# Performance work log

Measured on AMD Instinct MI355X. Metric: run time of the kernel, lower is better.

Reference implementation:

```python
import jax, jax.numpy as jnp
import numpy as np

N_QUBITS = 12
N_LAYERS = 5
OUTPUT_DIM = 4
BATCH = 1024


def _apply_1q(state, U, q, n):
    # state: (B, 2^n) complex; U: (B, 2, 2) per-sample unitary on wire q
    B = state.shape[0]
    s = state.reshape(B, 2 ** q, 2, -1)
    s = jnp.einsum('bik,bakc->baic', U, s)
    return s.reshape(B, -1)


def _cnot(state, c, t, n):
    # CNOT with control wire c, target wire t (wire 0 = most significant bit)
    B = state.shape[0]
    s = state.reshape((B,) + (2,) * n)
    s0 = jax.lax.index_in_dim(s, 0, axis=1 + c, keepdims=True)
    s1 = jax.lax.index_in_dim(s, 1, axis=1 + c, keepdims=True)
    s1 = jnp.flip(s1, axis=1 + t)  # X on target where control = 1
    return jnp.concatenate([s0, s1], axis=1 + c).reshape(B, -1)


def _forward(x, input_weights, theta, output_weights):
    n, L, D = N_QUBITS, N_LAYERS, OUTPUT_DIM
    x = jnp.tanh(x)
    B = x.shape[0]
    # |0...0> initial state, batched
    state = jnp.zeros((B, 2 ** n), jnp.complex64).at[:, 0].set(1.0)
    for l in range(L):
        # data re-uploading: RX(input_weights[l,j] * x[:,j]) on every wire, every layer
        a = input_weights[l][None, :] * x          # (B, n) RX angles
        b = theta[l, :, 0]                          # (n,) RY angles
        c = theta[l, :, 1]                          # (n,) RZ angles
        ca = jnp.cos(a / 2).astype(jnp.complex64)
        sa = jnp.sin(a / 2).astype(jnp.complex64)
        Rx = jnp.stack([jnp.stack([ca, -1j * sa], -1),
                        jnp.stack([-1j * sa, ca], -1)], -2)  # (B, n, 2, 2)
        cb = jnp.cos(b / 2).astype(jnp.complex64)
        sb = jnp.sin(b / 2).astype(jnp.complex64)
        ec = jnp.exp(-1j * c.astype(jnp.complex64) / 2)      # e^{-i c/2}
        # M = RZ(c) @ RY(b), shared across the batch
        M = jnp.stack([jnp.stack([ec * cb, -ec * sb], -1),
                       jnp.stack([jnp.conj(ec) * sb, jnp.conj(ec) * cb], -1)], -2)  # (n,2,2)
        # fused single-qubit unitary U = RZ @ RY @ RX per (sample, wire)
        U = jnp.einsum('qik,bqkj->bqij', M, Rx)
        for q in range(n):
            state = _apply_1q(state, U[:, q], q, n)
        for i in range(n):
            state = _cnot(state, i, (i + 1) % n, n)
    # exact <Z_i> on the first D wires
    p = jnp.abs(state) ** 2  # (B, 2^n)
    zs = []
    for i in range(D):
        pr = p.reshape(B, 2 ** i, 2, -1)
        zs.append(pr[:, :, 0, :].sum((1, 2)) - pr[:, :, 1, :].sum((1, 2)))
    Q = jnp.stack(zs, axis=1)  # (B, D)
    return output_weights[None, :] * Q


def setup_inputs() -> dict:
    key = jax.random.key(0)
    k1, k2, k3, k4 = jax.random.split(key, 4)
    return {
        'x': jax.random.normal(k1, (BATCH, N_QUBITS), jnp.float32),
        'input_weights': jax.random.normal(k2, (N_LAYERS, N_QUBITS), jnp.float32),
        'theta': jax.random.normal(k3, (N_LAYERS, N_QUBITS, 2), jnp.float32),
        'output_weights': jax.random.normal(k4, (OUTPUT_DIM,), jnp.float32),
    }


def reference(x, input_weights, theta, output_weights):
    return _forward(x, input_weights, theta, output_weights)
```

## Files before the change

kernel.cpp:

```cpp
#include <hip/hip_runtime.h>

#define NQ 12
#define NL 5
#define TPB 256

__host__ __device__ constexpr int sfx12_(int x) {
    x ^= x >> 1; x ^= x >> 2; x ^= x >> 4; x ^= x >> 8;
    return x & 0xFFF;
}
__host__ __device__ constexpr int par_(int x) {
    int y = x; y ^= y >> 8; y ^= y >> 4; y ^= y >> 2; y ^= y >> 1;
    return y & 1;
}
__host__ __device__ constexpr int amp_addr(int i) {
    const int g = i >> 1;
    const int G = g ^ ((g >> 3) & 7);
    return (G << 4) | ((i & 1) << 3);
}
__host__ __device__ constexpr int scat_c(int m) {
    const int s = sfx12_(m << 8);
    return amp_addr(s ^ ((s & 1) << 11));
}
__host__ __device__ constexpr int bpat(int m) { return amp_addr(m << 4); }
__host__ __device__ constexpr int meas_h(int m) {
    const int d = sfx12_(m << 8) ^ (par_(m) << 11);
    return (d >> 8) & 15;
}

__device__ __forceinline__ void gate_pair(float2 &a, float2 &c,
        const float2 u00, const float2 u01, const float2 u10, const float2 u11) {
    float2 n0, n1;
    n0.x = fmaf(u00.x, a.x, fmaf(-u00.y, a.y, fmaf(u01.x, c.x, -u01.y * c.y)));
    n0.y = fmaf(u00.x, a.y, fmaf( u00.y, a.x, fmaf(u01.x, c.y,  u01.y * c.x)));
    n1.x = fmaf(u10.x, a.x, fmaf(-u10.y, a.y, fmaf(u11.x, c.x, -u11.y * c.y)));
    n1.y = fmaf(u10.x, a.y, fmaf( u10.y, a.x, fmaf(u11.x, c.y,  u11.y * c.x)));
    a = n0; c = n1;
}
template <int K>
__device__ __forceinline__ void apply_gate(float2 (&v)[16], const float2* __restrict__ Uq) {
    const float2 u00 = Uq[0], u01 = Uq[1], u10 = Uq[2], u11 = Uq[3];
#pragma unroll
    for (int h = 0; h < 8; ++h) {
        const int m0 = ((h >> K) << (K + 1)) | (h & ((1 << K) - 1));
        gate_pair(v[m0], v[m0 | (1 << K)], u00, u01, u10, u11);
    }
}

extern "C" __global__ void __launch_bounds__(TPB)
qnet_kernel(const float* __restrict__ x, const float* __restrict__ iw,
            const float* __restrict__ th, const float* __restrict__ ow,
            float* __restrict__ out) {
    __shared__ float2 st[4096];
    __shared__ __align__(16) float2 U[NL][NQ][4];
    __shared__ float wz[4][4];
    char* stb = (char*)st;

    const int b = blockIdx.x;
    const int tid = threadIdx.x;
    const int w = tid >> 6;

    if (tid < NL * NQ) {
        const int l = tid / NQ, q = tid % NQ;
        const float xv = tanhf(x[b * NQ + q]);
        const float a = iw[l * NQ + q] * xv;
        const float bt = th[(l * NQ + q) * 2 + 0];
        const float ct = th[(l * NQ + q) * 2 + 1];
        float sa, ca; sincosf(0.5f * a, &sa, &ca);
        float sb, cb; sincosf(0.5f * bt, &sb, &cb);
        float sc, cc; sincosf(0.5f * ct, &sc, &cc);
        const float M00r = cc * cb, M00i = -sc * cb;
        const float M01r = -cc * sb, M01i = sc * sb;
        const float M10r = cc * sb, M10i = sc * sb;
        const float M11r = cc * cb, M11i = sc * cb;
        U[l][q][0] = make_float2(fmaf(M00r, ca,  sa * M01i), fmaf(M00i, ca, -sa * M01r));
        U[l][q][1] = make_float2(fmaf(ca, M01r,  sa * M00i), fmaf(ca, M01i, -sa * M00r));
        U[l][q][2] = make_float2(fmaf(M10r, ca,  sa * M11i), fmaf(M10i, ca, -sa * M11r));
        U[l][q][3] = make_float2(fmaf(ca, M11r,  sa * M10i), fmaf(ca, M11i, -sa * M10r));
    }

    const int baseA = amp_addr(tid << 4);
    const int baseB = amp_addr(((tid >> 4) << 8) | (tid & 15));
    const int baseC = amp_addr(tid);
    const int pt = __popc(tid) & 1;
    const int baseS = amp_addr(sfx12_(tid) ^ (pt << 11));
    const int hT = pt << 3;

    __syncthreads();

    float2 v[16];
#pragma unroll 1
    for (int l = 0; l < NL; ++l) {
        if (l == 0) {
#pragma unroll
            for (int r = 0; r < 16; ++r) v[r] = make_float2(0.f, 0.f);
            if (tid == 0) v[0].x = 1.f;
        } else {
#pragma unroll
            for (int c = 0; c < 8; ++c) {
                const float4 f = *(const float4*)(stb + (baseA ^ (c << 4)));
                v[2 * c]     = make_float2(f.x, f.y);
                v[2 * c + 1] = make_float2(f.z, f.w);
            }
        }
        apply_gate<0>(v, U[l][11]);
        apply_gate<1>(v, U[l][10]);
        apply_gate<2>(v, U[l][9]);
        apply_gate<3>(v, U[l][8]);
#pragma unroll
        for (int c = 0; c < 8; ++c)
            *(float4*)(stb + (baseA ^ (c << 4))) =
                make_float4(v[2 * c].x, v[2 * c].y, v[2 * c + 1].x, v[2 * c + 1].y);
        __syncthreads();

#pragma unroll
        for (int m = 0; m < 16; ++m)
            v[m] = *(const float2*)(stb + (baseB ^ bpat(m)));
        apply_gate<0>(v, U[l][7]);
        apply_gate<1>(v, U[l][6]);
        apply_gate<2>(v, U[l][5]);
        apply_gate<3>(v, U[l][4]);
#pragma unroll
        for (int m = 0; m < 16; ++m)
            *(float2*)(stb + (baseB ^ bpat(m))) = v[m];
        __syncthreads();

#pragma unroll
        for (int m = 0; m < 16; ++m)
            v[m] = *(const float2*)(stb + baseC + (m << 11));
        apply_gate<0>(v, U[l][3]);
        apply_gate<1>(v, U[l][2]);
        apply_gate<2>(v, U[l][1]);
        apply_gate<3>(v, U[l][0]);

        if (l != NL - 1) {
            __syncthreads();
#pragma unroll
            for (int m = 0; m < 16; ++m)
                *(float2*)(stb + (baseS ^ scat_c(m))) = v[m];
            __syncthreads();
        }
    }

    float z0 = 0.f, z1 = 0.f, z2 = 0.f, z3 = 0.f;
#pragma unroll
    for (int m = 0; m < 16; ++m) {
        const float pr = fmaf(v[m].x, v[m].x, v[m].y * v[m].y);
        const int h = meas_h(m) ^ hT;
        z0 += (h & 8) ? -pr : pr;
        z1 += (h & 4) ? -pr : pr;
        z2 += (h & 2) ? -pr : pr;
        z3 += (h & 1) ? -pr : pr;
    }
#pragma unroll
    for (int off = 32; off > 0; off >>= 1) {
        z0 += __shfl_xor(z0, off);
        z1 += __shfl_xor(z1, off);
        z2 += __shfl_xor(z2, off);
        z3 += __shfl_xor(z3, off);
    }
    if ((tid & 63) == 0) {
        wz[w][0] = z0; wz[w][1] = z1; wz[w][2] = z2; wz[w][3] = z3;
    }
    __syncthreads();
    if (tid < 4) {
        const float z = wz[0][tid] + wz[1][tid] + wz[2][tid] + wz[3][tid];
        out[b * 4 + tid] = ow[tid] * z;
    }
}

extern "C" void kernel_launch(void* const* d_in, const int* in_sizes, int n_in,
                              void* d_out, int out_size, void* d_ws, size_t ws_size,
                              hipStream_t stream) {
    const float* x  = (const float*)d_in[0];
    const float* iw = (const float*)d_in[1];
    const float* th = (const float*)d_in[2];
    const float* ow = (const float*)d_in[3];
    float* out = (float*)d_out;
    const int batch = in_sizes[0] / NQ;
    hipLaunchKernelGGL(qnet_kernel, dim3(batch), dim3(TPB), 0, stream,
                       x, iw, th, ow, out);
}
```

Measured before the change: 50.34 us.

## Use one wavefront per sample with 64 amplitudes per lane and two exchange passes

Shrinks each block to a single 64-thread wavefront that holds 64 amplitudes per lane. Six qubits are applied per register pass, so each layer needs two LDS exchange passes instead of three plus a scatter. Because the whole state lives in one wave, all __syncthreads calls and the cross-wave reduction are removed, and the LDS swizzle and the CNOT scatter and measurement patterns are adjusted to the new mapping. The cost is much higher register use and fewer waves per CU, which leaves less latency hiding and depends on in-order LDS access within a wavefront.

```diff
diff --git a/kernel.cpp b/kernel.cpp
--- a/kernel.cpp
+++ b/kernel.cpp
@@ -2,7 +2,7 @@
 
 #define NQ 12
 #define NL 5
-#define TPB 256
+#define TPB 64
 
 __host__ __device__ constexpr int sfx12_(int x) {
     x ^= x >> 1; x ^= x >> 2; x ^= x >> 4; x ^= x >> 8;
@@ -14,18 +14,13 @@
 }
 __host__ __device__ constexpr int amp_addr(int i) {
     const int g = i >> 1;
-    const int G = g ^ ((g >> 3) & 7);
+    const int G = g ^ ((g >> 5) & 7);
     return (G << 4) | ((i & 1) << 3);
 }
-__host__ __device__ constexpr int scat_c(int m) {
-    const int s = sfx12_(m << 8);
-    return amp_addr(s ^ ((s & 1) << 11));
-}
-__host__ __device__ constexpr int bpat(int m) { return amp_addr(m << 4); }
-__host__ __device__ constexpr int meas_h(int m) {
-    const int d = sfx12_(m << 8) ^ (par_(m) << 11);
-    return (d >> 8) & 15;
-}
+__host__ __device__ constexpr int fi_(int x) { return sfx12_(x) ^ (par_(x) << 11); }
+__host__ __device__ constexpr int mpat(int m) { return amp_addr(m << 6); }
+__host__ __device__ constexpr int spat(int m) { return amp_addr(fi_(m << 6)); }
+__host__ __device__ constexpr int mh_(int m) { return (fi_(m << 6) >> 8) & 15; }
 
 __device__ __forceinline__ void gate_pair(float2 &a, float2 &c,
         const float2 u00, const float2 u01, const float2 u10, const float2 u11) {
@@ -37,13 +32,14 @@
     a = n0; c = n1;
 }
 template <int K>
-__device__ __forceinline__ void apply_gate(float2 (&v)[16], const float2* __restrict__ Uq) {
+__device__ __forceinline__ void apply_gate(float2 (&v)[64], const float2* __restrict__ Uq) {
     const float2 u00 = Uq[0], u01 = Uq[1], u10 = Uq[2], u11 = Uq[3];
 #pragma unroll
-    for (int h = 0; h < 8; ++h) {
+    for (int h = 0; h < 32; ++h) {
         const int m0 = ((h >> K) << (K + 1)) | (h & ((1 << K) - 1));
         gate_pair(v[m0], v[m0 | (1 << K)], u00, u01, u10, u11);
     }
+    __builtin_amdgcn_sched_barrier(0);
 }
 
 extern "C" __global__ void __launch_bounds__(TPB)
@@ -52,12 +48,10 @@
             float* __restrict__ out) {
     __shared__ float2 st[4096];
     __shared__ __align__(16) float2 U[NL][NQ][4];
-    __shared__ float wz[4][4];
     char* stb = (char*)st;
 
     const int b = blockIdx.x;
     const int tid = threadIdx.x;
-    const int w = tid >> 6;
 
     if (tid < NL * NQ) {
         const int l = tid / NQ, q = tid % NQ;
@@ -78,25 +72,22 @@
         U[l][q][3] = make_float2(fmaf(ca, M11r,  sa * M10i), fmaf(ca, M11i, -sa * M10r));
     }
 
-    const int baseA = amp_addr(tid << 4);
-    const int baseB = amp_addr(((tid >> 4) << 8) | (tid & 15));
-    const int baseC = amp_addr(tid);
+    const int baseA = amp_addr(tid << 6);
+    const int baseB = amp_addr(tid);
     const int pt = __popc(tid) & 1;
-    const int baseS = amp_addr(sfx12_(tid) ^ (pt << 11));
+    const int baseS = amp_addr(fi_(tid));
     const int hT = pt << 3;
 
-    __syncthreads();
-
-    float2 v[16];
+    float2 v[64];
 #pragma unroll 1
     for (int l = 0; l < NL; ++l) {
         if (l == 0) {
 #pragma unroll
-            for (int r = 0; r < 16; ++r) v[r] = make_float2(0.f, 0.f);
+            for (int r = 0; r < 64; ++r) v[r] = make_float2(0.f, 0.f);
             if (tid == 0) v[0].x = 1.f;
         } else {
 #pragma unroll
-            for (int c = 0; c < 8; ++c) {
+            for (int c = 0; c < 32; ++c) {
                 const float4 f = *(const float4*)(stb + (baseA ^ (c << 4)));
                 v[2 * c]     = make_float2(f.x, f.y);
                 v[2 * c + 1] = make_float2(f.z, f.w);
@@ -106,46 +97,34 @@
         apply_gate<1>(v, U[l][10]);
         apply_gate<2>(v, U[l][9]);
         apply_gate<3>(v, U[l][8]);
+        apply_gate<4>(v, U[l][7]);
+        apply_gate<5>(v, U[l][6]);
 #pragma unroll
-        for (int c = 0; c < 8; ++c)
+        for (int c = 0; c < 32; ++c)
             *(float4*)(stb + (baseA ^ (c << 4))) =
                 make_float4(v[2 * c].x, v[2 * c].y, v[2 * c + 1].x, v[2 * c + 1].y);
-        __syncthreads();
 
 #pragma unroll
-        for (int m = 0; m < 16; ++m)
-            v[m] = *(const float2*)(stb + (baseB ^ bpat(m)));
-        apply_gate<0>(v, U[l][7]);
-        apply_gate<1>(v, U[l][6]);
-        apply_gate<2>(v, U[l][5]);
-        apply_gate<3>(v, U[l][4]);
+        for (int m = 0; m < 64; ++m)
+            v[m] = *(const float2*)(stb + (baseB ^ mpat(m)));
+        apply_gate<0>(v, U[l][5]);
+        apply_gate<1>(v, U[l][4]);
+        apply_gate<2>(v, U[l][3]);
+        apply_gate<3>(v, U[l][2]);
+        apply_gate<4>(v, U[l][1]);
+        apply_gate<5>(v, U[l][0]);
+        if (l != NL - 1) {
 #pragma unroll
-        for (int m = 0; m < 16; ++m)
-            *(float2*)(stb + (baseB ^ bpat(m))) = v[m];
-        __syncthreads();
-
-#pragma unroll
-        for (int m = 0; m < 16; ++m)
-            v[m] = *(const float2*)(stb + baseC + (m << 11));
-        apply_gate<0>(v, U[l][3]);
-        apply_gate<1>(v, U[l][2]);
-        apply_gate<2>(v, U[l][1]);
-        apply_gate<3>(v, U[l][0]);
-
-        if (l != NL - 1) {
-            __syncthreads();
-#pragma unroll
-            for (int m = 0; m < 16; ++m)
-                *(float2*)(stb + (baseS ^ scat_c(m))) = v[m];
-            __syncthreads();
+            for (int m = 0; m < 64; ++m)
+                *(float2*)(stb + (baseS ^ spat(m))) = v[m];
         }
     }
 
     float z0 = 0.f, z1 = 0.f, z2 = 0.f, z3 = 0.f;
 #pragma unroll
-    for (int m = 0; m < 16; ++m) {
+    for (int m = 0; m < 64; ++m) {
         const float pr = fmaf(v[m].x, v[m].x, v[m].y * v[m].y);
-        const int h = meas_h(m) ^ hT;
+        const int h = mh_(m) ^ hT;
         z0 += (h & 8) ? -pr : pr;
         z1 += (h & 4) ? -pr : pr;
         z2 += (h & 2) ? -pr : pr;
@@ -158,13 +137,9 @@
         z2 += __shfl_xor(z2, off);
         z3 += __shfl_xor(z3, off);
     }
-    if ((tid & 63) == 0) {
-        wz[w][0] = z0; wz[w][1] = z1; wz[w][2] = z2; wz[w][3] = z3;
-    }
-    __syncthreads();
-    if (tid < 4) {
-        const float z = wz[0][tid] + wz[1][tid] + wz[2][tid] + wz[3][tid];
-        out[b * 4 + tid] = ow[tid] * z;
+    if (tid == 0) {
+        const float4 o = make_float4(ow[0] * z0, ow[1] * z1, ow[2] * z2, ow[3] * z3);
+        *(float4*)(out + b * 4) = o;
     }
 }
 
```

Result: slower. 56.69 us (+12.6%).

## Precompute per-sample gate unitaries in separate kernel, read from global memory

Applied to the files above, without the earlier changes.

Moves the per-sample gate matrix computation (tanh, sincos, complex products) out of the simulator kernel into a new prep_gates kernel that writes all unitaries to workspace. The simulator then reads gate coefficients straight from global memory as uniform scalar loads and fully unrolls the layer loop. This drops one barrier and the serialized trig prologue inside each block, but adds a second kernel launch and a round trip of about 2 MB through global memory.

```diff
diff --git a/kernel.cpp b/kernel.cpp
--- a/kernel.cpp
+++ b/kernel.cpp
@@ -3,6 +3,7 @@
 #define NQ 12
 #define NL 5
 #define TPB 256
+#define NGATES (NL * NQ)
 
 __host__ __device__ constexpr int sfx12_(int x) {
     x ^= x >> 1; x ^= x >> 2; x ^= x >> 4; x ^= x >> 8;
@@ -37,8 +38,11 @@
     a = n0; c = n1;
 }
 template <int K>
-__device__ __forceinline__ void apply_gate(float2 (&v)[16], const float2* __restrict__ Uq) {
-    const float2 u00 = Uq[0], u01 = Uq[1], u10 = Uq[2], u11 = Uq[3];
+__device__ __forceinline__ void apply_gate(float2 (&v)[16], const float* __restrict__ g) {
+    const float2 u00 = make_float2(g[0], g[1]);
+    const float2 u01 = make_float2(g[2], g[3]);
+    const float2 u10 = make_float2(g[4], g[5]);
+    const float2 u11 = make_float2(g[6], g[7]);
 #pragma unroll
     for (int h = 0; h < 8; ++h) {
         const int m0 = ((h >> K) << (K + 1)) | (h & ((1 << K) - 1));
@@ -46,37 +50,45 @@
     }
 }
 
+extern "C" __global__ void __launch_bounds__(256)
+prep_gates(const float* __restrict__ x, const float* __restrict__ iw,
+           const float* __restrict__ th, float* __restrict__ Ug, int total) {
+    const int idx = blockIdx.x * 256 + threadIdx.x;
+    if (idx >= total) return;
+    const int b = idx / NGATES;
+    const int r = idx % NGATES;
+    const int l = r / NQ, q = r % NQ;
+    const float xv = tanhf(x[b * NQ + q]);
+    const float a = iw[l * NQ + q] * xv;
+    const float bt = th[(l * NQ + q) * 2 + 0];
+    const float ct = th[(l * NQ + q) * 2 + 1];
+    float sa, ca; sincosf(0.5f * a, &sa, &ca);
+    float sb, cb; sincosf(0.5f * bt, &sb, &cb);
+    float sc, cc; sincosf(0.5f * ct, &sc, &cc);
+    const float M00r = cc * cb, M00i = -sc * cb;
+    const float M01r = -cc * sb, M01i = sc * sb;
+    const float M10r = cc * sb, M10i = sc * sb;
+    const float M11r = cc * cb, M11i = sc * cb;
+    float4 lo, hi;
+    lo.x = fmaf(M00r, ca,  sa * M01i); lo.y = fmaf(M00i, ca, -sa * M01r);
+    lo.z = fmaf(ca, M01r,  sa * M00i); lo.w = fmaf(ca, M01i, -sa * M00r);
+    hi.x = fmaf(M10r, ca,  sa * M11i); hi.y = fmaf(M10i, ca, -sa * M11r);
+    hi.z = fmaf(ca, M11r,  sa * M10i); hi.w = fmaf(ca, M11i, -sa * M10r);
+    *(float4*)(Ug + idx * 8)     = lo;
+    *(float4*)(Ug + idx * 8 + 4) = hi;
+}
+
 extern "C" __global__ void __launch_bounds__(TPB)
-qnet_kernel(const float* __restrict__ x, const float* __restrict__ iw,
-            const float* __restrict__ th, const float* __restrict__ ow,
+qnet_kernel(const float* __restrict__ Ug, const float* __restrict__ ow,
             float* __restrict__ out) {
     __shared__ float2 st[4096];
-    __shared__ __align__(16) float2 U[NL][NQ][4];
     __shared__ float wz[4][4];
     char* stb = (char*)st;
 
     const int b = blockIdx.x;
     const int tid = threadIdx.x;
     const int w = tid >> 6;
-
-    if (tid < NL * NQ) {
-        const int l = tid / NQ, q = tid % NQ;
-        const float xv = tanhf(x[b * NQ + q]);
-        const float a = iw[l * NQ + q] * xv;
-        const float bt = th[(l * NQ + q) * 2 + 0];
-        const float ct = th[(l * NQ + q) * 2 + 1];
-        float sa, ca; sincosf(0.5f * a, &sa, &ca);
-        float sb, cb; sincosf(0.5f * bt, &sb, &cb);
-        float sc, cc; sincosf(0.5f * ct, &sc, &cc);
-        const float M00r = cc * cb, M00i = -sc * cb;
-        const float M01r = -cc * sb, M01i = sc * sb;
-        const float M10r = cc * sb, M10i = sc * sb;
-        const float M11r = cc * cb, M11i = sc * cb;
-        U[l][q][0] = make_float2(fmaf(M00r, ca,  sa * M01i), fmaf(M00i, ca, -sa * M01r));
-        U[l][q][1] = make_float2(fmaf(ca, M01r,  sa * M00i), fmaf(ca, M01i, -sa * M00r));
-        U[l][q][2] = make_float2(fmaf(M10r, ca,  sa * M11i), fmaf(M10i, ca, -sa * M11r));
-        U[l][q][3] = make_float2(fmaf(ca, M11r,  sa * M10i), fmaf(ca, M11i, -sa * M10r));
-    }
+    const float* __restrict__ Ub = Ug + b * (NGATES * 8);
 
     const int baseA = amp_addr(tid << 4);
     const int baseB = amp_addr(((tid >> 4) << 8) | (tid & 15));
@@ -85,11 +97,10 @@
     const int baseS = amp_addr(sfx12_(tid) ^ (pt << 11));
     const int hT = pt << 3;
 
-    __syncthreads();
-
     float2 v[16];
-#pragma unroll 1
+#pragma unroll
     for (int l = 0; l < NL; ++l) {
+        const float* __restrict__ Ul = Ub + l * (NQ * 8);
         if (l == 0) {
 #pragma unroll
             for (int r = 0; r < 16; ++r) v[r] = make_float2(0.f, 0.f);
@@ -102,10 +113,10 @@
                 v[2 * c + 1] = make_float2(f.z, f.w);
             }
         }
-        apply_gate<0>(v, U[l][11]);
-        apply_gate<1>(v, U[l][10]);
-        apply_gate<2>(v, U[l][9]);
-        apply_gate<3>(v, U[l][8]);
+        apply_gate<0>(v, Ul + 11 * 8);
+        apply_gate<1>(v, Ul + 10 * 8);
+        apply_gate<2>(v, Ul + 9 * 8);
+        apply_gate<3>(v, Ul + 8 * 8);
 #pragma unroll
         for (int c = 0; c < 8; ++c)
             *(float4*)(stb + (baseA ^ (c << 4))) =
@@ -115,10 +126,10 @@
 #pragma unroll
         for (int m = 0; m < 16; ++m)
             v[m] = *(const float2*)(stb + (baseB ^ bpat(m)));
-        apply_gate<0>(v, U[l][7]);
-        apply_gate<1>(v, U[l][6]);
-        apply_gate<2>(v, U[l][5]);
-        apply_gate<3>(v, U[l][4]);
+        apply_gate<0>(v, Ul + 7 * 8);
+        apply_gate<1>(v, Ul + 6 * 8);
+        apply_gate<2>(v, Ul + 5 * 8);
+        apply_gate<3>(v, Ul + 4 * 8);
 #pragma unroll
         for (int m = 0; m < 16; ++m)
             *(float2*)(stb + (baseB ^ bpat(m))) = v[m];
@@ -127,10 +138,10 @@
 #pragma unroll
         for (int m = 0; m < 16; ++m)
             v[m] = *(const float2*)(stb + baseC + (m << 11));
-        apply_gate<0>(v, U[l][3]);
-        apply_gate<1>(v, U[l][2]);
-        apply_gate<2>(v, U[l][1]);
-        apply_gate<3>(v, U[l][0]);
+        apply_gate<0>(v, Ul + 3 * 8);
+        apply_gate<1>(v, Ul + 2 * 8);
+        apply_gate<2>(v, Ul + 1 * 8);
+        apply_gate<3>(v, Ul + 0 * 8);
 
         if (l != NL - 1) {
             __syncthreads();
@@ -177,6 +188,10 @@
     const float* ow = (const float*)d_in[3];
     float* out = (float*)d_out;
     const int batch = in_sizes[0] / NQ;
+    float* Ug = (float*)d_ws;
+    const int total = batch * NGATES;
+    hipLaunchKernelGGL(prep_gates, dim3((total + 255) / 256), dim3(256), 0, stream,
+                       x, iw, th, Ug, total);
     hipLaunchKernelGGL(qnet_kernel, dim3(batch), dim3(TPB), 0, stream,
-                       x, iw, th, ow, out);
+                       Ug, ow, out);
 }
```

Result: faster. 48.82 us (-3.0%).

## Compute layer-0 state analytically as product state and measure from permuted buffer

Applied to the files above, without the earlier changes.

Layer 0 starts from |0...0>, so after its single-qubit gates and the CNOT ring the state is a permuted product state. The kernel now builds each thread's 16 amplitudes directly from products of U columns instead of running three gate passes with shared-memory round trips. The measurement is also restructured: the last layer scatters to shared memory like the others, then reads back in layout A so the Z signs come straight from thread-id bits. This removes about a fifth of the gate work and two barriers, but adds one scatter and a shared read at the end, and depends on the index permutation being derived correctly.

```diff
diff --git a/kernel.cpp b/kernel.cpp
--- a/kernel.cpp
+++ b/kernel.cpp
@@ -7,10 +7,6 @@
 __host__ __device__ constexpr int sfx12_(int x) {
     x ^= x >> 1; x ^= x >> 2; x ^= x >> 4; x ^= x >> 8;
     return x & 0xFFF;
-}
-__host__ __device__ constexpr int par_(int x) {
-    int y = x; y ^= y >> 8; y ^= y >> 4; y ^= y >> 2; y ^= y >> 1;
-    return y & 1;
 }
 __host__ __device__ constexpr int amp_addr(int i) {
     const int g = i >> 1;
@@ -22,11 +18,10 @@
     return amp_addr(s ^ ((s & 1) << 11));
 }
 __host__ __device__ constexpr int bpat(int m) { return amp_addr(m << 4); }
-__host__ __device__ constexpr int meas_h(int m) {
-    const int d = sfx12_(m << 8) ^ (par_(m) << 11);
-    return (d >> 8) & 15;
-}
-
+
+__device__ __forceinline__ float2 cmul(float2 a, float2 b) {
+    return make_float2(fmaf(a.x, b.x, -a.y * b.y), fmaf(a.x, b.y, a.y * b.x));
+}
 __device__ __forceinline__ void gate_pair(float2 &a, float2 &c,
         const float2 u00, const float2 u01, const float2 u10, const float2 u11) {
     float2 n0, n1;
@@ -83,18 +78,46 @@
     const int baseC = amp_addr(tid);
     const int pt = __popc(tid) & 1;
     const int baseS = amp_addr(sfx12_(tid) ^ (pt << 11));
-    const int hT = pt << 3;
 
     __syncthreads();
 
     float2 v[16];
-#pragma unroll 1
-    for (int l = 0; l < NL; ++l) {
-        if (l == 0) {
-#pragma unroll
-            for (int r = 0; r < 16; ++r) v[r] = make_float2(0.f, 0.f);
-            if (tid == 0) v[0].x = 1.f;
-        } else {
+    {
+        const int t0 = tid & 1, t1 = (tid >> 1) & 1, t2 = (tid >> 2) & 1, t3 = (tid >> 3) & 1;
+        const int t4 = (tid >> 4) & 1, t5 = (tid >> 5) & 1, t6 = (tid >> 6) & 1, t7 = (tid >> 7) & 1;
+        #define C0(k, bit) (U[0][11 - (k)][(bit) ? 2 : 0])
+        float2 Pm = cmul(C0(4, t0 ^ t1), C0(5, t1 ^ t2));
+        Pm = cmul(Pm, C0(6, t2 ^ t3));
+        Pm = cmul(Pm, C0(7, t3 ^ t4));
+        Pm = cmul(Pm, C0(8, t4 ^ t5));
+        Pm = cmul(Pm, C0(9, t5 ^ t6));
+        float2 P3[2];
+        P3[0] = cmul(Pm, C0(3, t0));
+        P3[1] = cmul(Pm, C0(3, 1 ^ t0));
+        float2 H[2];
+        H[0] = cmul(C0(10, t6 ^ t7), C0(11, t7));
+        H[1] = cmul(C0(10, t6 ^ t7 ^ 1), C0(11, t7 ^ 1));
+        float2 PH[2][2];
+        PH[0][0] = cmul(H[0], P3[0]); PH[0][1] = cmul(H[0], P3[1]);
+        PH[1][0] = cmul(H[1], P3[0]); PH[1][1] = cmul(H[1], P3[1]);
+        float2 T01[2][2];
+        T01[0][0] = cmul(C0(0, 0), C0(1, 0)); T01[0][1] = cmul(C0(0, 0), C0(1, 1));
+        T01[1][0] = cmul(C0(0, 1), C0(1, 0)); T01[1][1] = cmul(C0(0, 1), C0(1, 1));
+        float2 L8[8];
+#pragma unroll
+        for (int jj = 0; jj < 8; ++jj)
+            L8[jj] = cmul(T01[jj & 1][(jj >> 1) & 1], C0(2, (jj >> 2) & 1));
+        #undef C0
+#pragma unroll
+        for (int r = 0; r < 16; ++r) {
+            const int r0 = r & 1, r1 = (r >> 1) & 1, r2 = (r >> 2) & 1, r3 = (r >> 3) & 1;
+            v[r] = cmul(L8[(r0 ^ r1) | ((r1 ^ r2) << 1) | ((r2 ^ r3) << 2)], PH[r0][r3]);
+        }
+    }
+
+#pragma unroll
+    for (int l = 1; l < NL; ++l) {
+        if (l > 1) {
 #pragma unroll
             for (int c = 0; c < 8; ++c) {
                 const float4 f = *(const float4*)(stb + (baseA ^ (c << 4)));
@@ -131,35 +154,32 @@
         apply_gate<1>(v, U[l][2]);
         apply_gate<2>(v, U[l][1]);
         apply_gate<3>(v, U[l][0]);
-
-        if (l != NL - 1) {
-            __syncthreads();
-#pragma unroll
-            for (int m = 0; m < 16; ++m)
-                *(float2*)(stb + (baseS ^ scat_c(m))) = v[m];
-            __syncthreads();
-        }
-    }
-
-    float z0 = 0.f, z1 = 0.f, z2 = 0.f, z3 = 0.f;
-#pragma unroll
-    for (int m = 0; m < 16; ++m) {
-        const float pr = fmaf(v[m].x, v[m].x, v[m].y * v[m].y);
-        const int h = meas_h(m) ^ hT;
-        z0 += (h & 8) ? -pr : pr;
-        z1 += (h & 4) ? -pr : pr;
-        z2 += (h & 2) ? -pr : pr;
-        z3 += (h & 1) ? -pr : pr;
-    }
+        __syncthreads();
+#pragma unroll
+        for (int m = 0; m < 16; ++m)
+            *(float2*)(stb + (baseS ^ scat_c(m))) = v[m];
+        __syncthreads();
+    }
+
+    float ps = 0.f;
+#pragma unroll
+    for (int c = 0; c < 8; ++c) {
+        const float4 f = *(const float4*)(stb + (baseA ^ (c << 4)));
+        ps = fmaf(f.x, f.x, fmaf(f.y, f.y, fmaf(f.z, f.z, fmaf(f.w, f.w, ps))));
+    }
+    float s0 = (tid & 128) ? -ps : ps;
+    float s1 = (tid & 64) ? -ps : ps;
+    float s2 = (tid & 32) ? -ps : ps;
+    float s3 = (tid & 16) ? -ps : ps;
 #pragma unroll
     for (int off = 32; off > 0; off >>= 1) {
-        z0 += __shfl_xor(z0, off);
-        z1 += __shfl_xor(z1, off);
-        z2 += __shfl_xor(z2, off);
-        z3 += __shfl_xor(z3, off);
+        s0 += __shfl_xor(s0, off);
+        s1 += __shfl_xor(s1, off);
+        s2 += __shfl_xor(s2, off);
+        s3 += __shfl_xor(s3, off);
     }
     if ((tid & 63) == 0) {
-        wz[w][0] = z0; wz[w][1] = z1; wz[w][2] = z2; wz[w][3] = z3;
+        wz[w][0] = s0; wz[w][1] = s1; wz[w][2] = s2; wz[w][3] = s3;
     }
     __syncthreads();
     if (tid < 4) {
```

New measurement: 42.01 us. 1.2x faster.
